# Kernel tuning notes

Hardware: AMD Instinct MI355X
Metric: run time of the kernel (lower is better)

## Reference

```python
import jax, jax.numpy as jnp
import numpy as np

P_DROP = 0.3
TEMP = 1.0
UNC_THRESH = 0.3
TOP_K = 2
EXTRA_K = 2  # min(2, num_experts - top_k)
NUM_SAMPLES = 5


def setup_inputs() -> dict:
    key = jax.random.key(0)
    ks = jax.random.split(key, 7)
    B, D, H, E = 16384, 4096, 128, 64
    return {
        "x": jax.random.normal(ks[0], (B, D), jnp.float32),
        "W1": jax.random.normal(ks[1], (D, H), jnp.float32) / np.sqrt(D),
        "b1": jnp.zeros((H,), jnp.float32),
        "W2": jax.random.normal(ks[2], (H, E), jnp.float32) / np.sqrt(H),
        "b2": jnp.zeros((E,), jnp.float32),
        "mask1_u": jax.random.uniform(ks[3], (NUM_SAMPLES, B, H), jnp.float32),
        "mask2_u": jax.random.uniform(ks[4], (NUM_SAMPLES, B, E), jnp.float32),
    }


def reference(x, W1, b1, W2, b2, mask1_u, mask2_u):
    scale = 1.0 / (1.0 - P_DROP)
    # layer1: Linear -> ReLU -> Dropout; W1 is shared, so compute once and
    # apply per-sample dropout masks (identical math to the torch loop).
    h = jax.nn.relu(x @ W1 + b1)                              # [B, H]
    h = h[None] * ((mask1_u >= P_DROP).astype(h.dtype) * scale)  # [S, B, H]
    # layer2: Linear -> Dropout
    logits = jnp.einsum("sbh,he->sbe", h, W2) + b2            # [S, B, E]
    logits = logits * ((mask2_u >= P_DROP).astype(logits.dtype) * scale)

    mean_logits = logits.mean(axis=0)                          # [B, E]
    probs = jax.nn.softmax(mean_logits / TEMP, axis=-1)        # [B, E]
    all_probs = jax.nn.softmax(logits / TEMP, axis=-1)         # [S, B, E]
    # torch .std() is unbiased (ddof=1)
    uncertainty = jnp.std(all_probs, axis=0, ddof=1).mean(axis=-1)  # [B]

    # top_k + conditional expansion by EXTRA_K when uncertain.
    full_probs, full_idx = jax.lax.top_k(probs, TOP_K + EXTRA_K)
    topk_probs, topk_idx = full_probs[:, :TOP_K], full_idx[:, :TOP_K]
    uncertain = (uncertainty > UNC_THRESH)[:, None]
    extra_probs = jnp.where(uncertain, full_probs[:, TOP_K:], 0.0)
    extra_idx = jnp.where(uncertain, full_idx[:, TOP_K:], -1)
    out_idx = jnp.concatenate([topk_idx, extra_idx], axis=1)       # [B, TOP_K+EXTRA_K]
    out_probs = jnp.concatenate([topk_probs, extra_probs], axis=1)
    return out_idx, out_probs, uncertainty
```

## Files before the change

### kernel.cpp

```cpp
#include <hip/hip_runtime.h>

typedef short short8 __attribute__((ext_vector_type(8)));
typedef float f32x4 __attribute__((ext_vector_type(4)));

#define B_ROWS 16384
#define SCALE 1.4285714285714286f

__device__ __forceinline__ float bf2f(unsigned short u) {
    return __uint_as_float(((unsigned)u) << 16);
}
__device__ __forceinline__ unsigned short f2bf(float f) {
    unsigned u = __float_as_uint(f);
    u += 0x7fffu + ((u >> 16) & 1u);
    return (unsigned short)(u >> 16);
}

__device__ __forceinline__ void gl_lds16(const void* g, void* l) {
    __builtin_amdgcn_global_load_lds(
        (const __attribute__((address_space(1))) unsigned int*)g,
        (__attribute__((address_space(3))) unsigned int*)l, 16, 0, 0);
}

__device__ __forceinline__ float wave_max(float v) {
    #pragma unroll
    for (int m = 1; m < 64; m <<= 1) v = fmaxf(v, __shfl_xor(v, m, 64));
    return v;
}
__device__ __forceinline__ float wave_sum(float v) {
    #pragma unroll
    for (int m = 1; m < 64; m <<= 1) v += __shfl_xor(v, m, 64);
    return v;
}

__global__ void k_prep(const float* __restrict__ w1,
                       unsigned short* __restrict__ w1h,
                       unsigned short* __restrict__ w1l) {
    int tid = blockIdx.x * 256 + threadIdx.x;
    int n = tid >> 12, k = tid & 4095;
    float v = w1[k * 128 + n];
    unsigned short hi = f2bf(v);
    w1h[tid] = hi;
    w1l[tid] = f2bf(v - bf2f(hi));
}

struct A2 { float4 a, b; };

__global__ __launch_bounds__(512, 1) void k_gemm(
        const float* __restrict__ x,
        const unsigned short* __restrict__ w1h,
        const unsigned short* __restrict__ w1l,
        const float* __restrict__ b1,
        float* __restrict__ hout) {
    __shared__ __attribute__((aligned(128))) char smem[131072];
    unsigned short* sBh0 = (unsigned short*)smem;
    unsigned short* sBl0 = (unsigned short*)(smem + 49152);
    unsigned short* sAh0 = (unsigned short*)(smem + 98304);
    unsigned short* sAl0 = (unsigned short*)(smem + 114688);

    const int t = threadIdx.x;
    const int w = t >> 6, lane = t & 63;
    const int l15 = lane & 15, l4 = lane >> 4;
    const int cg = w & 3, rg = w >> 2;
    const int rowBase = blockIdx.x << 6;

    const int am = t >> 3;
    const int rem = t & 7;
    const int aDst = ((am << 3) + (rem ^ (am & 7))) << 3;

    f32x4 acc[2][2];
    #pragma unroll
    for (int mf = 0; mf < 2; ++mf)
        #pragma unroll
        for (int nf = 0; nf < 2; ++nf) {
            f32x4 z = {0.f, 0.f, 0.f, 0.f};
            acc[mf][nf] = z;
        }

    auto stageB = [&](int bbuf, int k0) {
        #pragma unroll
        for (int j = 0; j < 2; ++j) {
            int c = (j << 9) + t;
            int n = c >> 3;
            int cl = (c & 7) ^ (n & 7);
            const size_t go = (size_t)n * 4096 + k0 + (cl << 3);
            gl_lds16(w1h + go, sBh0 + (bbuf << 13) + (c << 3));
            gl_lds16(w1l + go, sBl0 + (bbuf << 13) + (c << 3));
        }
    };
    auto loadA = [&](int k0) {
        const float* src = x + ((size_t)(rowBase + am) << 12) + k0 + (rem << 3);
        A2 r;
        r.a = *(const float4*)src;
        r.b = *(const float4*)(src + 4);
        return r;
    };
    auto writeA = [&](int abuf, A2 v) {
        float av[8] = {v.a.x, v.a.y, v.a.z, v.a.w, v.b.x, v.b.y, v.b.z, v.b.w};
        short8 H, L;
        #pragma unroll
        for (int i = 0; i < 8; ++i) {
            unsigned short hi = f2bf(av[i]);
            H[i] = (short)hi;
            L[i] = (short)f2bf(av[i] - bf2f(hi));
        }
        *(short8*)(sAh0 + (abuf << 12) + aDst) = H;
        *(short8*)(sAl0 + (abuf << 12) + aDst) = L;
    };
    auto compute = [&](int abuf, int bbuf) {
        #pragma unroll
        for (int ks = 0; ks < 2; ++ks) {
            short8 ah[2], al[2], bh[2], bl[2];
            #pragma unroll
            for (int mf = 0; mf < 2; ++mf) {
                int rm = (rg << 5) + (mf << 4) + l15;
                int pc = ((ks << 2) + l4) ^ (rm & 7);
                int o = ((rm << 3) + pc) << 3;
                ah[mf] = *(const short8*)(sAh0 + (abuf << 12) + o);
                al[mf] = *(const short8*)(sAl0 + (abuf << 12) + o);
            }
            #pragma unroll
            for (int nf = 0; nf < 2; ++nf) {
                int rn = (cg << 5) + (nf << 4) + l15;
                int pc = ((ks << 2) + l4) ^ (rn & 7);
                int o = ((rn << 3) + pc) << 3;
                bh[nf] = *(const short8*)(sBh0 + (bbuf << 13) + o);
                bl[nf] = *(const short8*)(sBl0 + (bbuf << 13) + o);
            }
            #pragma unroll
            for (int mf = 0; mf < 2; ++mf)
                #pragma unroll
                for (int nf = 0; nf < 2; ++nf) {
                    acc[mf][nf] = __builtin_amdgcn_mfma_f32_16x16x32_bf16(
                        ah[mf], bh[nf], acc[mf][nf], 0, 0, 0);
                    acc[mf][nf] = __builtin_amdgcn_mfma_f32_16x16x32_bf16(
                        ah[mf], bl[nf], acc[mf][nf], 0, 0, 0);
                    acc[mf][nf] = __builtin_amdgcn_mfma_f32_16x16x32_bf16(
                        al[mf], bh[nf], acc[mf][nf], 0, 0, 0);
                }
        }
    };
    #define SOFTBAR() do { \
        asm volatile("s_waitcnt lgkmcnt(0)" ::: "memory"); \
        __builtin_amdgcn_s_barrier(); } while (0)

    int rb0 = 0, rb1 = 1, rb2 = 2;
    stageB(0, 0);
    stageB(1, 64);
    A2 P = loadA(0);
    A2 Q = loadA(64);
    writeA(0, P);
    __syncthreads();

    for (int m = 0; m < 31; ++m) {
        const int kE = (2 * m + 2) << 6;
        const int kO = (2 * m + 3) << 6;
        stageB(rb2, kE);
        P = loadA(kE);
        writeA(1, Q);
        compute(0, rb0);
        SOFTBAR();
        { int tb = rb0; rb0 = rb1; rb1 = rb2; rb2 = tb; }
        stageB(rb2, kO);
        Q = loadA(kO);
        writeA(0, P);
        compute(1, rb0);
        SOFTBAR();
        { int tb = rb0; rb0 = rb1; rb1 = rb2; rb2 = tb; }
    }
    writeA(1, Q);
    compute(0, rb0);
    SOFTBAR();
    { int tb = rb0; rb0 = rb1; rb1 = rb2; rb2 = tb; }
    compute(1, rb0);

    #pragma unroll
    for (int nf = 0; nf < 2; ++nf) {
        const int col = (cg << 5) + (nf << 4) + l15;
        const float bias = b1[col];
        #pragma unroll
        for (int mf = 0; mf < 2; ++mf) {
            const int rbase = (rg << 5) + (mf << 4) + (l4 << 2);
            #pragma unroll
            for (int rr = 0; rr < 4; ++rr) {
                const int r = rowBase + rbase + rr;
                float v = acc[mf][nf][rr] + bias;
                hout[(size_t)r * 128 + col] = v > 0.f ? v : 0.f;
            }
        }
    }
    #undef SOFTBAR
}

__global__ __launch_bounds__(512, 2) void k_logstats(
        const float* __restrict__ hg,
        const float* __restrict__ w2,
        const float* __restrict__ b2,
        const float* __restrict__ m1,
        const float* __restrict__ m2,
        float* __restrict__ out) {
    __shared__ __attribute__((aligned(128))) char smem[65536];
    float* hmb = (float*)smem;
    float* w2s = (float*)(smem + 32768);
    float* lgs = (float*)smem;

    const int t = threadIdx.x;
    const int w = t >> 6, lane = t & 63;
    const int lr = t >> 4;
    const int eg = t & 15;
    const int e0 = eg << 2;
    const int rowBase = blockIdx.x << 5;
    const int row = rowBase + lr;
    const int lsw = (lr & 7) << 2;

    float acc2[5][4];
    #pragma unroll
    for (int s = 0; s < 5; ++s)
        #pragma unroll
        for (int e = 0; e < 4; ++e) acc2[s][e] = 0.f;

    auto stage_hm = [&](int slot, int sidx) {
        #pragma unroll
        for (int j = 0; j < 2; ++j) {
            int q = t + (j << 9);
            int r = q >> 5, kq = q & 31;
            size_t gidx = ((size_t)(rowBase + r)) << 7;
            float4 mu = *(const float4*)(m1 + (size_t)sidx * (B_ROWS * 128)
                                            + gidx + (kq << 2));
            float4 h4 = *(const float4*)(hg + gidx + (kq << 2));
            float4 hm4;
            hm4.x = (mu.x >= 0.3f) ? h4.x * SCALE : 0.f;
            hm4.y = (mu.y >= 0.3f) ? h4.y * SCALE : 0.f;
            hm4.z = (mu.z >= 0.3f) ? h4.z * SCALE : 0.f;
            hm4.w = (mu.w >= 0.3f) ? h4.w * SCALE : 0.f;
            *(float4*)(hmb + (slot << 12) + r * 128 + ((kq << 2) ^ ((r & 7) << 2))) = hm4;
        }
    };

    #pragma unroll
    for (int j = 0; j < 4; ++j) {
        int q = t + (j << 9);
        *(float4*)(w2s + (q << 2)) = *(const float4*)(w2 + (q << 2));
    }
    stage_hm(0, 0);
    stage_hm(1, 1);
    __syncthreads();

    for (int p = 0; p < 3; ++p) {
        const int s0 = p << 1;
        const int ns = (p == 2) ? 1 : 2;
        const float* hm0 = hmb + lr * 128;
        const float* hm1 = hmb + 4096 + lr * 128;
        for (int kq = 0; kq < 32; ++kq) {
            const int hoff = (kq << 2) ^ lsw;
            float4 a0 = *(const float4*)(hm0 + hoff);
            float ha[4] = {a0.x, a0.y, a0.z, a0.w};
            float w2v[4][4];
            #pragma unroll
            for (int kk = 0; kk < 4; ++kk) {
                float4 wa = *(const float4*)(w2s + (((kq << 2) + kk) << 6) + e0);
                w2v[kk][0] = wa.x; w2v[kk][1] = wa.y; w2v[kk][2] = wa.z; w2v[kk][3] = wa.w;
            }
            #pragma unroll
            for (int kk = 0; kk < 4; ++kk)
                #pragma unroll
                for (int e = 0; e < 4; ++e)
                    acc2[s0][e] += ha[kk] * w2v[kk][e];
            if (ns == 2) {
                float4 a1 = *(const float4*)(hm1 + hoff);
                float hb[4] = {a1.x, a1.y, a1.z, a1.w};
                #pragma unroll
                for (int kk = 0; kk < 4; ++kk)
                    #pragma unroll
                    for (int e = 0; e < 4; ++e)
                        acc2[s0 + 1][e] += hb[kk] * w2v[kk][e];
            }
        }
        __syncthreads();
        if (p < 2) {
            stage_hm(0, (p << 1) + 2);
            if (p == 0) stage_hm(1, 3);
            __syncthreads();
        }
    }

    {
        float4 ba = *(const float4*)(b2 + e0);
        float bv4[4] = {ba.x, ba.y, ba.z, ba.w};
        #pragma unroll
        for (int s = 0; s < 5; ++s) {
            const float* m2p = m2 + ((size_t)s * B_ROWS + row) * 64 + e0;
            float4 ma = *(const float4*)m2p;
            float mk[4] = {ma.x, ma.y, ma.z, ma.w};
            float lv[4];
            #pragma unroll
            for (int e = 0; e < 4; ++e) {
                float v = acc2[s][e] + bv4[e];
                lv[e] = (mk[e] >= 0.3f) ? v * SCALE : 0.f;
            }
            *(float4*)(lgs + ((s << 5) + lr) * 64 + e0) =
                make_float4(lv[0], lv[1], lv[2], lv[3]);
        }
    }
    __syncthreads();

    for (int r4 = 0; r4 < 4; ++r4) {
        const int r = (w << 2) + r4;
        float l[5], p[5];
        #pragma unroll
        for (int s = 0; s < 5; ++s)
            l[s] = lgs[((s << 5) + r) * 64 + lane];

        float ml = ((((l[0] + l[1]) + l[2]) + l[3]) + l[4]) / 5.0f;

        #pragma unroll
        for (int s = 0; s < 5; ++s) {
            float mx = wave_max(l[s]);
            float ev = expf(l[s] - mx);
            float sm = wave_sum(ev);
            p[s] = ev / sm;
        }

        float mx = wave_max(ml);
        float ev = expf(ml - mx);
        float sm = wave_sum(ev);
        float prob = ev / sm;

        float mean = ((((p[0] + p[1]) + p[2]) + p[3]) + p[4]) / 5.0f;
        float var = 0.f;
        #pragma unroll
        for (int s = 0; s < 5; ++s) { float d = p[s] - mean; var += d * d; }
        float sd = sqrtf(var * 0.25f);
        float unc = wave_sum(sd) / 64.0f;

        float pv = prob;
        float vv[4]; int vi[4];
        #pragma unroll
        for (int q = 0; q < 4; ++q) {
            float bvx = pv; int bi = lane;
            #pragma unroll
            for (int m = 1; m < 64; m <<= 1) {
                float ov = __shfl_xor(bvx, m, 64);
                int oi = __shfl_xor(bi, m, 64);
                if (ov > bvx || (ov == bvx && oi < bi)) { bvx = ov; bi = oi; }
            }
            vv[q] = bvx; vi[q] = bi;
            if (lane == bi) pv = -1.f;
        }

        if (lane == 0) {
            int grow = rowBase + r;
            bool ug = unc > 0.3f;
            float4 fi = make_float4((float)vi[0], (float)vi[1],
                                    ug ? (float)vi[2] : -1.f,
                                    ug ? (float)vi[3] : -1.f);
            *(float4*)(out + (size_t)grow * 4) = fi;
            float4 fp = make_float4(vv[0], vv[1],
                                    ug ? vv[2] : 0.f,
                                    ug ? vv[3] : 0.f);
            *(float4*)(out + 65536 + (size_t)grow * 4) = fp;
            out[131072 + grow] = unc;
        }
    }
}

extern "C" void kernel_launch(void* const* d_in, const int* in_sizes, int n_in,
                              void* d_out, int out_size, void* d_ws, size_t ws_size,
                              hipStream_t stream) {
    const float* x  = (const float*)d_in[0];
    const float* W1 = (const float*)d_in[1];
    const float* b1 = (const float*)d_in[2];
    const float* W2 = (const float*)d_in[3];
    const float* b2 = (const float*)d_in[4];
    const float* m1 = (const float*)d_in[5];
    const float* m2 = (const float*)d_in[6];
    float* out = (float*)d_out;
    char* ws = (char*)d_ws;

    unsigned short* w1h = (unsigned short*)ws;
    unsigned short* w1l = (unsigned short*)(ws + (1 << 20));
    float* h = (float*)(ws + (2 << 20));

    k_prep    <<<2048, 256, 0, stream>>>(W1, w1h, w1l);
    k_gemm    <<<256,  512, 0, stream>>>(x, w1h, w1l, b1, h);
    k_logstats<<<512,  512, 0, stream>>>(h, W2, b2, m1, m2, out);
}
```

Measured before the change: 483.1 us.

## Deepen x prefetch to four k-tiles and rotate k order per block

The GEMM main loop now loads four consecutive 64-wide k-tiles of x per thread in one batch, instead of one tile ahead. It uses explicit vmcnt waits so each compute step waits only for the data it needs, keeping more global loads in flight. Each block also starts its k traversal at a block-dependent offset, for both the W1 staging and the x loads, to spread concurrent memory traffic across addresses. The cost is more registers for the prefetched group, some redundant wrap-around loads in the final iteration, and hand-tuned wait counts that must match the exact number of issued loads.

New measurement: 471.7 us. 2.3% less time.

```diff
diff --git a/kernel.cpp b/kernel.cpp
--- a/kernel.cpp
+++ b/kernel.cpp
@@ -43,7 +43,7 @@
     w1l[tid] = f2bf(v - bf2f(hi));
 }
 
-struct A2 { float4 a, b; };
+struct Grp { float4 a0, a1, b0, b1, c0, c1, d0, d1; };
 
 __global__ __launch_bounds__(512, 1) void k_gemm(
         const float* __restrict__ x,
@@ -62,6 +62,7 @@
     const int l15 = lane & 15, l4 = lane >> 4;
     const int cg = w & 3, rg = w >> 2;
     const int rowBase = blockIdx.x << 6;
+    const int rot4 = blockIdx.x & 15;
 
     const int am = t >> 3;
     const int rem = t & 7;
@@ -76,7 +77,8 @@
             acc[mf][nf] = z;
         }
 
-    auto stageB = [&](int bbuf, int k0) {
+    auto stageB = [&](int bbuf, int T) {
+        const int k0 = ((T + (rot4 << 2)) & 63) << 6;
         #pragma unroll
         for (int j = 0; j < 2; ++j) {
             int c = (j << 9) + t;
@@ -87,24 +89,27 @@
             gl_lds16(w1l + go, sBl0 + (bbuf << 13) + (c << 3));
         }
     };
-    auto loadA = [&](int k0) {
-        const float* src = x + ((size_t)(rowBase + am) << 12) + k0 + (rem << 3);
-        A2 r;
-        r.a = *(const float4*)src;
-        r.b = *(const float4*)(src + 4);
+    auto loadGroup = [&](int g) {
+        const float* rp = x + ((size_t)(rowBase + am) << 12)
+                            + (((g + rot4) & 15) << 8) + (rem << 3);
+        Grp r;
+        r.a0 = *(const float4*)(rp);       r.a1 = *(const float4*)(rp + 4);
+        r.b0 = *(const float4*)(rp + 64);  r.b1 = *(const float4*)(rp + 68);
+        r.c0 = *(const float4*)(rp + 128); r.c1 = *(const float4*)(rp + 132);
+        r.d0 = *(const float4*)(rp + 192); r.d1 = *(const float4*)(rp + 196);
         return r;
     };
-    auto writeA = [&](int abuf, A2 v) {
-        float av[8] = {v.a.x, v.a.y, v.a.z, v.a.w, v.b.x, v.b.y, v.b.z, v.b.w};
-        short8 H, L;
+    auto writeA = [&](int abuf, float4 va, float4 vb) {
+        float av[8] = {va.x, va.y, va.z, va.w, vb.x, vb.y, vb.z, vb.w};
+        short8 Hh, Ll;
         #pragma unroll
         for (int i = 0; i < 8; ++i) {
             unsigned short hi = f2bf(av[i]);
-            H[i] = (short)hi;
-            L[i] = (short)f2bf(av[i] - bf2f(hi));
-        }
-        *(short8*)(sAh0 + (abuf << 12) + aDst) = H;
-        *(short8*)(sAl0 + (abuf << 12) + aDst) = L;
+            Hh[i] = (short)hi;
+            Ll[i] = (short)f2bf(av[i] - bf2f(hi));
+        }
+        *(short8*)(sAh0 + (abuf << 12) + aDst) = Hh;
+        *(short8*)(sAl0 + (abuf << 12) + aDst) = Ll;
     };
     auto compute = [&](int abuf, int bbuf) {
         #pragma unroll
@@ -139,39 +144,50 @@
                 }
         }
     };
+    #define VM12() asm volatile("s_waitcnt vmcnt(12)" ::: "memory")
+    #define VM4()  asm volatile("s_waitcnt vmcnt(4)"  ::: "memory")
     #define SOFTBAR() do { \
         asm volatile("s_waitcnt lgkmcnt(0)" ::: "memory"); \
         __builtin_amdgcn_s_barrier(); } while (0)
+    #define RINGROT() do { int tb = rb0; rb0 = rb1; rb1 = rb2; rb2 = tb; } while (0)
 
     int rb0 = 0, rb1 = 1, rb2 = 2;
     stageB(0, 0);
-    stageB(1, 64);
-    A2 P = loadA(0);
-    A2 Q = loadA(64);
-    writeA(0, P);
-    __syncthreads();
-
-    for (int m = 0; m < 31; ++m) {
-        const int kE = (2 * m + 2) << 6;
-        const int kO = (2 * m + 3) << 6;
-        stageB(rb2, kE);
-        P = loadA(kE);
-        writeA(1, Q);
-        compute(0, rb0);
-        SOFTBAR();
-        { int tb = rb0; rb0 = rb1; rb1 = rb2; rb2 = tb; }
-        stageB(rb2, kO);
-        Q = loadA(kO);
-        writeA(0, P);
-        compute(1, rb0);
-        SOFTBAR();
-        { int tb = rb0; rb0 = rb1; rb1 = rb2; rb2 = tb; }
-    }
-    writeA(1, Q);
-    compute(0, rb0);
+    stageB(1, 1);
+    Grp G = loadGroup(0);
+    Grp H;
+    writeA(0, G.a0, G.a1);
     SOFTBAR();
-    { int tb = rb0; rb0 = rb1; rb1 = rb2; rb2 = tb; }
-    compute(1, rb0);
+
+    for (int s8 = 0; s8 < 8; ++s8) {
+        const int T0 = s8 << 3;
+        stageB(rb2, T0 + 2);
+        H = loadGroup((T0 >> 2) + 1);
+        writeA(1, G.b0, G.b1);
+        VM12(); compute(0, rb0); SOFTBAR(); RINGROT();
+        stageB(rb2, T0 + 3);
+        writeA(0, G.c0, G.c1);
+        VM12(); compute(1, rb0); SOFTBAR(); RINGROT();
+        stageB(rb2, T0 + 4);
+        writeA(1, G.d0, G.d1);
+        VM4(); compute(0, rb0); SOFTBAR(); RINGROT();
+        stageB(rb2, T0 + 5);
+        writeA(0, H.a0, H.a1);
+        VM4(); compute(1, rb0); SOFTBAR(); RINGROT();
+        stageB(rb2, T0 + 6);
+        G = loadGroup((T0 >> 2) + 2);
+        writeA(1, H.b0, H.b1);
+        VM12(); compute(0, rb0); SOFTBAR(); RINGROT();
+        stageB(rb2, T0 + 7);
+        writeA(0, H.c0, H.c1);
+        VM12(); compute(1, rb0); SOFTBAR(); RINGROT();
+        stageB(rb2, T0 + 8);
+        writeA(1, H.d0, H.d1);
+        VM4(); compute(0, rb0); SOFTBAR(); RINGROT();
+        stageB(rb2, T0 + 9);
+        writeA(0, G.a0, G.a1);
+        VM4(); compute(1, rb0); SOFTBAR(); RINGROT();
+    }
 
     #pragma unroll
     for (int nf = 0; nf < 2; ++nf) {
@@ -188,7 +204,10 @@
             }
         }
     }
+    #undef VM12
+    #undef VM4
     #undef SOFTBAR
+    #undef RINGROT
 }
 
 __global__ __launch_bounds__(512, 2) void k_logstats(
```
